# Kernel optimization log

Hardware: AMD Instinct MI355X
Metric: run time of the kernel (lower is better)

## Reference

```python
import jax, jax.numpy as jnp
import numpy as np

SOS = 4998
EOS = 4999
SCALING = 2.0


def setup_inputs() -> dict:
    key = jax.random.key(0)
    ks = jax.random.split(key, 12)
    B, T, E, D, A, C, F, ODIM, L = 32, 1000, 512, 1024, 512, 10, 100, 5000, 100
    s = 0.02
    return {
        "hpad": jax.random.normal(ks[0], (B, T, E), jnp.float32),
        "ys": jax.random.randint(ks[1], (B, L), 0, SOS, jnp.int32),
        # AttLoc params
        "w_enc": jax.random.normal(ks[2], (A, E), jnp.float32) * s,
        "b_enc": jnp.zeros((A,), jnp.float32),
        "w_dec": jax.random.normal(ks[3], (A, D), jnp.float32) * s,
        "w_att": jax.random.normal(ks[4], (A, C), jnp.float32) * s,
        "w_conv": jax.random.normal(ks[5], (C, 1, 2 * F + 1), jnp.float32) * s,  # OIH 1D conv kernel
        "w_gvec": jax.random.normal(ks[6], (1, A), jnp.float32) * s,
        "b_gvec": jnp.zeros((1,), jnp.float32),
        # Decoder params
        "embed": jax.random.normal(ks[7], (ODIM, D), jnp.float32) * s,
        "w_ih": jax.random.normal(ks[8], (4 * D, D + E), jnp.float32) * s,
        "w_hh": jax.random.normal(ks[9], (4 * D, D), jnp.float32) * s,
        "b_ih": jnp.zeros((4 * D,), jnp.float32),
        "b_hh": jnp.zeros((4 * D,), jnp.float32),
        "w_out": jax.random.normal(ks[10], (ODIM, D), jnp.float32) * s,
        "b_out": jnp.zeros((ODIM,), jnp.float32),
    }


def _decode(hpad, ys, w_enc, b_enc, w_dec, w_att, w_conv, w_gvec, b_gvec,
            embed, w_ih, w_hh, b_ih, b_hh, w_out, b_out):
    B, T, E = hpad.shape
    D = w_hh.shape[1]
    F = (w_conv.shape[-1] - 1) // 2
    # ys_in = [sos; y] per utterance (all same length -> already padded)
    ys_in = jnp.concatenate([jnp.full((B, 1), SOS, ys.dtype), ys], axis=1)  # [B, olen]
    eys = embed[ys_in]                                                      # [B, olen, D]
    # pre_compute_enc_h = mlp_enc(enc_h)
    pre = jnp.einsum('bte,ae->bta', hpad, w_enc) + b_enc                    # [B, T, A]
    att0 = jnp.full((B, T), 1.0 / T, hpad.dtype)   # uniform init attention (all hlen == T)
    z0 = jnp.zeros((B, D), hpad.dtype)
    c0 = jnp.zeros((B, D), hpad.dtype)

    def step(carry, ey_i):
        z, c, aw = carry
        # location-aware conv over previous attention weights: [B,1,T] -> [B,C,T]
        conv = jax.lax.conv_general_dilated(aw[:, None, :], w_conv, (1,), [(F, F)],
                                            dimension_numbers=('NCH', 'OIH', 'NCH'))
        att_feat = jnp.einsum('bct,ac->bta', conv, w_att)                   # mlp_att
        dec = (z @ w_dec.T)[:, None, :]                                     # mlp_dec, tiled
        e = jnp.tanh(att_feat + pre + dec) @ w_gvec[0] + b_gvec[0]          # [B, T]
        w = jax.nn.softmax(SCALING * e, axis=1)
        ctx = jnp.einsum('bt,bte->be', w, hpad)                             # [B, E]
        # LSTMCell
        x = jnp.concatenate([ey_i, ctx], axis=1)                            # [B, D+E]
        gates = x @ w_ih.T + b_ih + z @ w_hh.T + b_hh
        i_g, f_g, g_g, o_g = jnp.split(gates, 4, axis=1)
        c_new = jax.nn.sigmoid(f_g) * c + jax.nn.sigmoid(i_g) * jnp.tanh(g_g)
        z_new = jax.nn.sigmoid(o_g) * jnp.tanh(c_new)
        return (z_new, c_new, w), z_new

    _, z_all = jax.lax.scan(step, (z0, c0, att0), jnp.swapaxes(eys, 0, 1))  # [olen, B, D]
    y_all = jnp.einsum('obd,vd->obv', z_all, w_out) + b_out                 # [olen, B, odim]
    return jnp.swapaxes(y_all, 0, 1)                                        # [B, olen, odim]


def reference(hpad, ys, w_enc, b_enc, w_dec, w_att, w_conv, w_gvec, b_gvec,
              embed, w_ih, w_hh, b_ih, b_hh, w_out, b_out):
    return _decode(hpad, ys, w_enc, b_enc, w_dec, w_att, w_conv, w_gvec, b_gvec,
                   embed, w_ih, w_hh, b_ih, b_hh, w_out, b_out)
```

## Files before the change

### kernel.cpp

```cpp
#include <hip/hip_runtime.h>
#include <math.h>

#define B_    32
#define T_    1000
#define E_    512
#define D_    1024
#define A_    512
#define C_    10
#define F_    100
#define ODIM_ 5000
#define OLEN_ 101
#define SOS_  4998

#define OFF_PRE   0u
#define N_PREF    (32u*512u*1000u/2u)
#define OFF_HPB   (OFF_PRE + N_PREF)
#define N_HPBF    (32u*1000u*512u/2u)
#define OFF_DEC   (OFF_HPB + N_HPBF)
#define N_DEC     (32u*512u)
#define OFF_CONV  (OFF_DEC + N_DEC)
#define N_CONVB   (32u*10u*1000u)
#define OFF_AW    (OFF_CONV + N_CONVB)
#define N_AW      (32u*1000u)
#define OFF_S     (OFF_AW + N_AW)
#define N_S       (64u)
#define OFF_CTX   (OFF_S + N_S)
#define N_CTX     (32u*512u)
#define OFF_GP    (OFF_CTX + N_CTX)
#define N_GP      (8u*32u*4096u)
#define OFF_Z     (OFF_GP + N_GP)
#define N_Z       (32u*1024u)
#define OFF_C     (OFF_Z + N_Z)
#define OFF_ZALL  (OFF_C + N_Z)

__device__ __forceinline__ float fast_tanh(float x) {
    float cx = fminf(8.f, fmaxf(-8.f, x));
    float e = __expf(2.f * cx);
    return (e - 1.f) * __builtin_amdgcn_rcpf(e + 1.f);
}
__device__ __forceinline__ float fast_sigmoid(float x) {
    float cx = fminf(30.f, fmaxf(-30.f, x));
    return __builtin_amdgcn_rcpf(1.f + __expf(-cx));
}

__device__ __forceinline__ unsigned bf16rne(float f) {
    unsigned u = __float_as_uint(f);
    return (u + 0x7fffu + ((u >> 16) & 1u)) >> 16;
}
__device__ __forceinline__ unsigned packbf(float lo, float hi) {
    return bf16rne(lo) | (bf16rne(hi) << 16);
}
__device__ __forceinline__ float bflo(unsigned u) { return __uint_as_float(u << 16); }
__device__ __forceinline__ float bfhi(unsigned u) { return __uint_as_float(u & 0xffff0000u); }

__global__ __launch_bounds__(256) void k_init(float* ws) {
    int i = blockIdx.x * 256 + threadIdx.x;
    if (i < (int)N_Z) { ws[OFF_Z + i] = 0.f; ws[OFF_C + i] = 0.f; }
    if (i < (int)N_CTX) ws[OFF_CTX + i] = 0.f;
    if (i < (int)N_AW) ws[OFF_AW + i] = 1.0f;
    if (i < 64) ws[OFF_S + i] = (i >= 32) ? 1000.f : 0.f;
}

__global__ __launch_bounds__(256) void k_hp16(const float* __restrict__ hp, float* ws) {
    uint2* hpb = (uint2*)(ws + OFF_HPB);
    const float4* src = (const float4*)hp;
    for (unsigned i = blockIdx.x * 256 + threadIdx.x; i < 4096000u; i += 4000u * 256u) {
        float4 v = src[i];
        uint2 o;
        o.x = packbf(v.x, v.y);
        o.y = packbf(v.z, v.w);
        hpb[i] = o;
    }
}

__global__ __launch_bounds__(256) void k_pre_t(const float* __restrict__ hp,
                                               const float* __restrict__ we,
                                               const float* __restrict__ be,
                                               float* ws) {
    __shared__ float As[64][68];
    __shared__ float Bs[64][68];
    unsigned short* preb = (unsigned short*)(ws + OFF_PRE);
    int bt = blockIdx.y;
    int b = bt >> 4, tc = bt & 15;
    int t0 = tc * 64;
    int n0 = blockIdx.x * 64;
    int tid = threadIdx.x;
    int tr = tid >> 4, tcl = tid & 15;
    float acc[4][4] = {};
    for (int k0 = 0; k0 < 512; k0 += 64) {
        for (int i = tid; i < 1024; i += 256) {
            int m = i >> 4, kq = (i & 15) << 2;
            int t = t0 + m;
            float4 v = (t < 1000) ? *(const float4*)&hp[((size_t)(b * 1000 + t)) * 512 + k0 + kq]
                                  : make_float4(0.f, 0.f, 0.f, 0.f);
            As[kq + 0][m] = v.x; As[kq + 1][m] = v.y; As[kq + 2][m] = v.z; As[kq + 3][m] = v.w;
            float4 w = *(const float4*)&we[(size_t)(n0 + m) * 512 + k0 + kq];
            Bs[kq + 0][m] = w.x; Bs[kq + 1][m] = w.y; Bs[kq + 2][m] = w.z; Bs[kq + 3][m] = w.w;
        }
        __syncthreads();
        #pragma unroll 16
        for (int kk = 0; kk < 64; ++kk) {
            float4 av = *(const float4*)&As[kk][tr << 2];
            float4 bv = *(const float4*)&Bs[kk][tcl << 2];
            float a[4] = {av.x, av.y, av.z, av.w};
            float bq[4] = {bv.x, bv.y, bv.z, bv.w};
            #pragma unroll
            for (int i = 0; i < 4; i++)
                #pragma unroll
                for (int j = 0; j < 4; j++) acc[i][j] += a[i] * bq[j];
        }
        __syncthreads();
    }
    int tt = t0 + (tr << 2);
    if (tt < 1000) {
        #pragma unroll
        for (int j = 0; j < 4; ++j) {
            int a = n0 + (tcl << 2) + j;
            float bea = be[a];
            uint2 o;
            o.x = packbf(acc[0][j] + bea, acc[1][j] + bea);
            o.y = packbf(acc[2][j] + bea, acc[3][j] + bea);
            *(uint2*)&preb[((size_t)(b * 512 + a)) * 1000 + tt] = o;
        }
    }
}

__global__ __launch_bounds__(256, 2) void k_prep(const float* __restrict__ wdec,
                                                 const float* __restrict__ wconv,
                                                 const float* __restrict__ wih,
                                                 const float* __restrict__ whh,
                                                 const float* __restrict__ embed,
                                                 const int* __restrict__ ys,
                                                 float* ws, int step) {
    int tid = threadIdx.x;
    if (blockIdx.x < 1024) {
        int u = blockIdx.x;
        if (u < 64) ws[OFF_CTX + u * 256 + tid] = 0.f;
        if (u == 64 && tid < 32) ws[OFF_S + (step & 1) * 32 + tid] = 0.f;
        int w = u * 4 + (tid >> 6);
        int lane = tid & 63;
        int a = w >> 3, bg7 = w & 7;
        const float4* wr = (const float4*)(wdec + (size_t)a * 1024);
        float4 w4[4];
        #pragma unroll
        for (int i = 0; i < 4; i++) w4[i] = wr[i * 64 + lane];
        float acc[4] = {0.f, 0.f, 0.f, 0.f};
        #pragma unroll
        for (int bb = 0; bb < 4; ++bb) {
            const float4* zr = (const float4*)(ws + OFF_Z + (size_t)(bg7 * 4 + bb) * 1024);
            #pragma unroll
            for (int i = 0; i < 4; i++) {
                float4 z4 = zr[i * 64 + lane];
                acc[bb] += w4[i].x * z4.x + w4[i].y * z4.y + w4[i].z * z4.z + w4[i].w * z4.w;
            }
        }
        #pragma unroll
        for (int off = 32; off > 0; off >>= 1) {
            acc[0] += __shfl_xor(acc[0], off, 64);
            acc[1] += __shfl_xor(acc[1], off, 64);
            acc[2] += __shfl_xor(acc[2], off, 64);
            acc[3] += __shfl_xor(acc[3], off, 64);
        }
        if (lane == 0) {
            #pragma unroll
            for (int bb = 0; bb < 4; ++bb)
                ws[OFF_DEC + (bg7 * 4 + bb) * 512 + a] = acc[bb];
        }
    } else if (blockIdx.x < 1344) {
        int blk = blockIdx.x - 1024;
        int b = blk / 10, c = blk - b * 10;
        if (tid >= 250) return;
        float invS = __builtin_amdgcn_rcpf(ws[OFF_S + ((step + 1) & 1) * 32 + b]);
        int t = tid * 4;
        const float* ar = ws + OFF_AW + b * 1000;
        const float* wc = wconv + c * 201;
        float a0, a1, a2, a3;
        a0 = (t - 100 >= 0) ? ar[t - 100] : 0.f;
        a1 = (t -  99 >= 0) ? ar[t -  99] : 0.f;
        a2 = (t -  98 >= 0) ? ar[t -  98] : 0.f;
        a3 = (t -  97 >= 0) ? ar[t -  97] : 0.f;
        float c0 = 0.f, c1 = 0.f, c2 = 0.f, c3 = 0.f;
        #pragma unroll 4
        for (int j = 0; j < 201; ++j) {
            float w = wc[j];
            c0 += a0 * w; c1 += a1 * w; c2 += a2 * w; c3 += a3 * w;
            a0 = a1; a1 = a2; a2 = a3;
            int ni = t + j - 96;
            a3 = (ni >= 0 && ni < 1000) ? ar[ni] : 0.f;
        }
        float* o = ws + OFF_CONV + (size_t)(b * 10 + c) * 1000 + t;
        o[0] = c0 * invS; o[1] = c1 * invS; o[2] = c2 * invS; o[3] = c3 * invS;
    } else {
        __shared__ float wlds[32][132];
        __shared__ float xs[32][36];
        int blk = blockIdx.x - 1344;
        int nt = blk & 31, ks = blk >> 5;
        int n0 = nt * 128;
        bool isE = (ks < 4);
        int kloc = isE ? ks * 256 : (ks - 4) * 256;
        int r = tid >> 1, h = tid & 1;
        int bx = tid >> 3, q8 = tid & 7;
        int tok = (step == 0) ? SOS_ : ys[bx * 100 + step - 1];
        const float* xsrc = isE ? (embed + (size_t)tok * 1024 + kloc)
                                : (ws + OFF_Z + (size_t)bx * 1024 + kloc);
        int nq = tid & 31, bq = tid >> 5;
        float acc[4][4] = {};
        for (int kc = 0; kc < 8; ++kc) {
            int koff = kc * 32;
            {
                const float* wrow = isE ? (wih + (size_t)(n0 + r) * 1536 + kloc + koff + h * 16)
                                        : (whh + (size_t)(n0 + r) * 1024 + kloc + koff + h * 16);
                #pragma unroll
                for (int j = 0; j < 4; ++j) {
                    float4 v = *(const float4*)&wrow[j * 4];
                    int kb = h * 16 + j * 4;
                    wlds[kb + 0][r] = v.x; wlds[kb + 1][r] = v.y;
                    wlds[kb + 2][r] = v.z; wlds[kb + 3][r] = v.w;
                }
            }
            {
                float4 v = *(const float4*)&xsrc[koff + q8 * 4];
                xs[q8 * 4 + 0][bx] = v.x; xs[q8 * 4 + 1][bx] = v.y;
                xs[q8 * 4 + 2][bx] = v.z; xs[q8 * 4 + 3][bx] = v.w;
            }
            __syncthreads();
            #pragma unroll 8
            for (int kk = 0; kk < 32; ++kk) {
                float4 wv = *(const float4*)&wlds[kk][nq * 4];
                float4 xv = *(const float4*)&xs[kk][bq * 4];
                float wa[4] = {wv.x, wv.y, wv.z, wv.w};
                float xa[4] = {xv.x, xv.y, xv.z, xv.w};
                #pragma unroll
                for (int i = 0; i < 4; i++)
                    #pragma unroll
                    for (int j = 0; j < 4; j++) acc[i][j] += wa[i] * xa[j];
            }
            __syncthreads();
        }
        float* gp = ws + OFF_GP + (size_t)(ks * 32 + bq * 4) * 4096 + n0 + nq * 4;
        #pragma unroll
        for (int j = 0; j < 4; j++)
            #pragma unroll
            for (int i = 0; i < 4; i++)
                gp[(size_t)j * 4096 + i] = acc[i][j];
    }
}

__global__ __launch_bounds__(512) void k_ectx(const float* __restrict__ watt,
                                              const float* __restrict__ gvec,
                                              const float* __restrict__ bgv,
                                              float* ws, int step) {
    __shared__ float part[1024];
    __shared__ float wsh[128];
    const unsigned short* preb = (const unsigned short*)(ws + OFF_PRE);
    const unsigned short* hpb  = (const unsigned short*)(ws + OFF_HPB);
    int b = blockIdx.x >> 3, tc = blockIdx.x & 7;
    int tbase = tc * 128;
    int tid = threadIdx.x;
    int w = tid >> 6, l = tid & 63;
    int t = tbase + l * 2;
    bool valid = (t < 1000);
    float2 cvv[10];
    const float* convb = ws + OFF_CONV + b * 10000;
    #pragma unroll
    for (int c = 0; c < 10; ++c)
        cvv[c] = valid ? *(const float2*)&convb[c * 1000 + t] : make_float2(0.f, 0.f);
    const float* decb = ws + OFF_DEC + b * 512;
    int a0 = w * 64;
    const unsigned short* pt = preb + ((size_t)(b * 512 + a0)) * 1000 + t;
    float ex = 0.f, ey = 0.f;
    #pragma unroll 8
    for (int a = a0; a < a0 + 64; ++a) {
        unsigned u = valid ? *(const unsigned*)pt : 0u;
        pt += 1000;
        float px = bflo(u), py = bfhi(u);
        float da = decb[a];
        float sx = px + da, sy = py + da;
        const float* wa = watt + a * 10;
        #pragma unroll
        for (int c = 0; c < 10; ++c) {
            float wv = wa[c];
            sx += cvv[c].x * wv; sy += cvv[c].y * wv;
        }
        float gva = gvec[a];
        ex += gva * fast_tanh(sx);
        ey += gva * fast_tanh(sy);
    }
    part[w * 128 + l * 2]     = ex;
    part[w * 128 + l * 2 + 1] = ey;
    __syncthreads();
    float wtil = 0.f;
    if (tid < 128) {
        int tt = tbase + tid;
        float e = 0.f;
        #pragma unroll
        for (int j = 0; j < 8; ++j) e += part[j * 128 + tid];
        if (tt < 1000) {
            wtil = __expf(2.f * (e + bgv[0]));
            ws[OFF_AW + b * 1000 + tt] = wtil;
        }
        wsh[tid] = wtil;
    }
    __syncthreads();
    part[tid] = wtil;
    __syncthreads();
    for (int off = 256; off >= 1; off >>= 1) {
        if (tid < off) part[tid] += part[tid + off];
        __syncthreads();
    }
    if (tid == 0) atomicAdd(&ws[OFF_S + (step & 1) * 32 + b], part[0]);
    int e4 = tid & 127, th = tid >> 7;
    int lt0 = th * 32;
    int ltend = lt0 + 32;
    int tmax = 1000 - tbase; if (ltend > tmax) ltend = tmax;
    float4 acc = make_float4(0.f, 0.f, 0.f, 0.f);
    for (int lt = lt0; lt < ltend; ++lt) {
        float wv = wsh[lt];
        uint2 hu = *(const uint2*)&hpb[((size_t)(b * 1000 + tbase + lt)) * 512 + e4 * 4];
        acc.x += wv * bflo(hu.x); acc.y += wv * bfhi(hu.x);
        acc.z += wv * bflo(hu.y); acc.w += wv * bfhi(hu.y);
    }
    float* cx = ws + OFF_CTX + b * 512 + e4 * 4;
    atomicAdd(cx + 0, acc.x); atomicAdd(cx + 1, acc.y);
    atomicAdd(cx + 2, acc.z); atomicAdd(cx + 3, acc.w);
}

__global__ __launch_bounds__(256, 2) void k_gl(const float* __restrict__ wih,
                                               const float* __restrict__ bih,
                                               const float* __restrict__ bhh,
                                               float* ws, int step) {
    __shared__ float wlds[32][36];
    __shared__ float xs[32][36];
    __shared__ float glb[32][33];
    __shared__ float sinv[32];
    int tid = threadIdx.x;
    int d0 = blockIdx.x * 8;
    if (tid < 32) sinv[tid] = __builtin_amdgcn_rcpf(ws[OFF_S + (step & 1) * 32 + tid]);
    __syncthreads();
    int r = tid >> 3, h = tid & 7;
    int ng_r = (r >> 3) * 1024 + d0 + (r & 7);
    const float* wrow = wih + (size_t)ng_r * 1536 + 1024 + h * 4;
    int bx = tid >> 3, q8 = tid & 7;
    const float* xsrc = ws + OFF_CTX + (size_t)bx * 512 + q8 * 4;
    float xscale = sinv[bx];
    int nq = tid & 15, bq = tid >> 4;
    float acc[2][2] = {};
    for (int kc = 0; kc < 16; ++kc) {
        int k0 = kc * 32;
        {
            float4 v = *(const float4*)&wrow[k0];
            wlds[h * 4 + 0][r] = v.x; wlds[h * 4 + 1][r] = v.y;
            wlds[h * 4 + 2][r] = v.z; wlds[h * 4 + 3][r] = v.w;
        }
        {
            float4 v = *(const float4*)&xsrc[k0];
            xs[q8 * 4 + 0][bx] = v.x * xscale; xs[q8 * 4 + 1][bx] = v.y * xscale;
            xs[q8 * 4 + 2][bx] = v.z * xscale; xs[q8 * 4 + 3][bx] = v.w * xscale;
        }
        __syncthreads();
        #pragma unroll 8
        for (int kk = 0; kk < 32; ++kk) {
            float w0 = wlds[kk][nq * 2], w1 = wlds[kk][nq * 2 + 1];
            float x0 = xs[kk][bq * 2],  x1 = xs[kk][bq * 2 + 1];
            acc[0][0] += w0 * x0; acc[0][1] += w0 * x1;
            acc[1][0] += w1 * x0; acc[1][1] += w1 * x1;
        }
        __syncthreads();
    }
    #pragma unroll
    for (int i = 0; i < 2; ++i) {
        int nl = nq * 2 + i;
        int ng = (nl >> 3) * 1024 + d0 + (nl & 7);
        float bb = bih[ng] + bhh[ng];
        #pragma unroll
        for (int j = 0; j < 2; ++j) {
            int b = bq * 2 + j;
            float s = acc[i][j] + bb;
            #pragma unroll
            for (int sl = 0; sl < 8; ++sl)
                s += ws[OFF_GP + (size_t)(sl * 32 + b) * 4096 + ng];
            glb[nl][b] = s;
        }
    }
    __syncthreads();
    {
        int dl = tid >> 5, b = tid & 31;
        float gi = glb[dl][b];
        float gf = glb[8 + dl][b];
        float gg = glb[16 + dl][b];
        float go = glb[24 + dl][b];
        int id = b * 1024 + d0 + dl;
        float c_old = ws[OFF_C + id];
        float si = fast_sigmoid(gi);
        float sf = fast_sigmoid(gf);
        float so = fast_sigmoid(go);
        float cn = sf * c_old + si * fast_tanh(gg);
        float hh = so * fast_tanh(cn);
        ws[OFF_C + id] = cn;
        ws[OFF_Z + id] = hh;
        ws[OFF_ZALL + ((size_t)step * 32 + b) * 1024 + d0 + dl] = hh;
    }
}

__global__ __launch_bounds__(256) void k_out(const float* __restrict__ zall,
                                             const float* __restrict__ wo,
                                             const float* __restrict__ bo,
                                             float* __restrict__ out) {
    __shared__ float As[64][68];
    __shared__ float Bs[64][68];
    int m0 = blockIdx.y * 64, n0 = blockIdx.x * 64;
    int tid = threadIdx.x;
    int tr = tid >> 4, tc = tid & 15;
    float acc[4][4] = {};
    for (int k0 = 0; k0 < 1024; k0 += 64) {
        for (int i = tid; i < 1024; i += 256) {
            int m = i >> 4, kq = (i & 15) << 2;
            int gm = m0 + m;
            float4 v = (gm < 3232) ? *(const float4*)&zall[(size_t)gm * 1024 + k0 + kq]
                                   : make_float4(0.f, 0.f, 0.f, 0.f);
            As[kq + 0][m] = v.x; As[kq + 1][m] = v.y; As[kq + 2][m] = v.z; As[kq + 3][m] = v.w;
            int gn = n0 + m;
            float4 w = (gn < 5000) ? *(const float4*)&wo[(size_t)gn * 1024 + k0 + kq]
                                   : make_float4(0.f, 0.f, 0.f, 0.f);
            Bs[kq + 0][m] = w.x; Bs[kq + 1][m] = w.y; Bs[kq + 2][m] = w.z; Bs[kq + 3][m] = w.w;
        }
        __syncthreads();
        #pragma unroll 16
        for (int kk = 0; kk < 64; ++kk) {
            float4 av = *(const float4*)&As[kk][tr << 2];
            float4 bv = *(const float4*)&Bs[kk][tc << 2];
            float a[4] = {av.x, av.y, av.z, av.w};
            float b[4] = {bv.x, bv.y, bv.z, bv.w};
            #pragma unroll
            for (int i = 0; i < 4; i++)
                #pragma unroll
                for (int j = 0; j < 4; j++) acc[i][j] += a[i] * b[j];
        }
        __syncthreads();
    }
    #pragma unroll
    for (int i = 0; i < 4; i++) {
        int m = m0 + (tr << 2) + i;
        if (m >= 3232) continue;
        int b = m & 31, o = m >> 5;
        #pragma unroll
        for (int j = 0; j < 4; j++) {
            int v = n0 + (tc << 2) + j;
            if (v < 5000)
                out[((size_t)b * 101 + o) * 5000 + v] = acc[i][j] + bo[v];
        }
    }
}

extern "C" void kernel_launch(void* const* d_in, const int* in_sizes, int n_in,
                              void* d_out, int out_size, void* d_ws, size_t ws_size,
                              hipStream_t stream) {
    const float* hpad   = (const float*)d_in[0];
    const int*   ys     = (const int*)d_in[1];
    const float* w_enc  = (const float*)d_in[2];
    const float* b_enc  = (const float*)d_in[3];
    const float* w_dec  = (const float*)d_in[4];
    const float* w_att  = (const float*)d_in[5];
    const float* w_conv = (const float*)d_in[6];
    const float* w_gvec = (const float*)d_in[7];
    const float* b_gvec = (const float*)d_in[8];
    const float* embed  = (const float*)d_in[9];
    const float* w_ih   = (const float*)d_in[10];
    const float* w_hh   = (const float*)d_in[11];
    const float* b_ih   = (const float*)d_in[12];
    const float* b_hh   = (const float*)d_in[13];
    const float* w_out  = (const float*)d_in[14];
    const float* b_out  = (const float*)d_in[15];
    float* ws  = (float*)d_ws;
    float* out = (float*)d_out;

    k_init<<<128, 256, 0, stream>>>(ws);
    k_hp16<<<4000, 256, 0, stream>>>(hpad, ws);
    k_pre_t<<<dim3(8, 512), 256, 0, stream>>>(hpad, w_enc, b_enc, ws);

    for (int step = 0; step < OLEN_; ++step) {
        k_prep<<<1600, 256, 0, stream>>>(w_dec, w_conv, w_ih, w_hh, embed, ys, ws, step);
        k_ectx<<<256, 512, 0, stream>>>(w_att, w_gvec, b_gvec, ws, step);
        k_gl<<<128, 256, 0, stream>>>(w_ih, b_ih, b_hh, ws, step);
    }

    k_out<<<dim3(79, 51), 256, 0, stream>>>(ws + OFF_ZALL, w_out, b_out, out);
}
```

Before: 10.38 ms.

## Stage attention weights in LDS and split LSTM gate kernel across more blocks

k_ectx now copies w_att, w_gvec and the decoder projection for the batch row into shared memory once per block, and the inner loop reads them as float4 from LDS instead of scalar global loads. Its launch bounds now request two blocks per CU. k_gl now handles 4 hidden units per block instead of 8 and launches 256 blocks, so the serial per-step gate GEMV is spread over more CUs. The cost is redundant ctx loading per block and half the threads idling in the LSTM cell update.

Result: no change. 10.19 ms (-1.9%).

```diff
diff --git a/kernel.cpp b/kernel.cpp
--- a/kernel.cpp
+++ b/kernel.cpp
@@ -246,10 +246,11 @@
     }
 }
 
-__global__ __launch_bounds__(512) void k_ectx(const float* __restrict__ watt,
-                                              const float* __restrict__ gvec,
-                                              const float* __restrict__ bgv,
-                                              float* ws, int step) {
+__global__ __launch_bounds__(512, 2) void k_ectx(const float* __restrict__ watt,
+                                                 const float* __restrict__ gvec,
+                                                 const float* __restrict__ bgv,
+                                                 float* ws, int step) {
+    __shared__ float sa[512 * 12];
     __shared__ float part[1024];
     __shared__ float wsh[128];
     const unsigned short* preb = (const unsigned short*)(ws + OFF_PRE);
@@ -257,6 +258,15 @@
     int b = blockIdx.x >> 3, tc = blockIdx.x & 7;
     int tbase = tc * 128;
     int tid = threadIdx.x;
+    {
+        const float* wrow = watt + tid * 10;
+        float* d = sa + tid * 12;
+        #pragma unroll
+        for (int c = 0; c < 10; ++c) d[c] = wrow[c];
+        d[10] = gvec[tid];
+        d[11] = ws[OFF_DEC + b * 512 + tid];
+    }
+    __syncthreads();
     int w = tid >> 6, l = tid & 63;
     int t = tbase + l * 2;
     bool valid = (t < 1000);
@@ -265,7 +275,6 @@
     #pragma unroll
     for (int c = 0; c < 10; ++c)
         cvv[c] = valid ? *(const float2*)&convb[c * 1000 + t] : make_float2(0.f, 0.f);
-    const float* decb = ws + OFF_DEC + b * 512;
     int a0 = w * 64;
     const unsigned short* pt = preb + ((size_t)(b * 512 + a0)) * 1000 + t;
     float ex = 0.f, ey = 0.f;
@@ -273,18 +282,24 @@
     for (int a = a0; a < a0 + 64; ++a) {
         unsigned u = valid ? *(const unsigned*)pt : 0u;
         pt += 1000;
+        const float4* sp = (const float4*)(sa + a * 12);
+        float4 w0 = sp[0];
+        float4 w1 = sp[1];
+        float4 w2 = sp[2];
         float px = bflo(u), py = bfhi(u);
-        float da = decb[a];
-        float sx = px + da, sy = py + da;
-        const float* wa = watt + a * 10;
-        #pragma unroll
-        for (int c = 0; c < 10; ++c) {
-            float wv = wa[c];
-            sx += cvv[c].x * wv; sy += cvv[c].y * wv;
-        }
-        float gva = gvec[a];
-        ex += gva * fast_tanh(sx);
-        ey += gva * fast_tanh(sy);
+        float sx = px + w2.w, sy = py + w2.w;
+        sx += cvv[0].x * w0.x; sy += cvv[0].y * w0.x;
+        sx += cvv[1].x * w0.y; sy += cvv[1].y * w0.y;
+        sx += cvv[2].x * w0.z; sy += cvv[2].y * w0.z;
+        sx += cvv[3].x * w0.w; sy += cvv[3].y * w0.w;
+        sx += cvv[4].x * w1.x; sy += cvv[4].y * w1.x;
+        sx += cvv[5].x * w1.y; sy += cvv[5].y * w1.y;
+        sx += cvv[6].x * w1.z; sy += cvv[6].y * w1.z;
+        sx += cvv[7].x * w1.w; sy += cvv[7].y * w1.w;
+        sx += cvv[8].x * w2.x; sy += cvv[8].y * w2.x;
+        sx += cvv[9].x * w2.y; sy += cvv[9].y * w2.y;
+        ex += w2.z * fast_tanh(sx);
+        ey += w2.z * fast_tanh(sy);
     }
     part[w * 128 + l * 2]     = ex;
     part[w * 128 + l * 2 + 1] = ey;
@@ -329,28 +344,28 @@
                                                const float* __restrict__ bih,
                                                const float* __restrict__ bhh,
                                                float* ws, int step) {
-    __shared__ float wlds[32][36];
-    __shared__ float xs[32][36];
-    __shared__ float glb[32][33];
+    __shared__ float wlds[32][20];
+    __shared__ float xs[32][33];
+    __shared__ float glb[16][33];
     __shared__ float sinv[32];
     int tid = threadIdx.x;
-    int d0 = blockIdx.x * 8;
+    int d0 = blockIdx.x * 4;
     if (tid < 32) sinv[tid] = __builtin_amdgcn_rcpf(ws[OFF_S + (step & 1) * 32 + tid]);
     __syncthreads();
-    int r = tid >> 3, h = tid & 7;
-    int ng_r = (r >> 3) * 1024 + d0 + (r & 7);
-    const float* wrow = wih + (size_t)ng_r * 1536 + 1024 + h * 4;
+    int r = tid >> 4, h = tid & 15;
+    int ng_r = (r >> 2) * 1024 + d0 + (r & 3);
+    const float* wrow = wih + (size_t)ng_r * 1536 + 1024 + h * 2;
     int bx = tid >> 3, q8 = tid & 7;
     const float* xsrc = ws + OFF_CTX + (size_t)bx * 512 + q8 * 4;
     float xscale = sinv[bx];
-    int nq = tid & 15, bq = tid >> 4;
-    float acc[2][2] = {};
+    int nq = tid & 7, bq = tid >> 3;
+    float acc[2] = {0.f, 0.f};
     for (int kc = 0; kc < 16; ++kc) {
         int k0 = kc * 32;
         {
-            float4 v = *(const float4*)&wrow[k0];
-            wlds[h * 4 + 0][r] = v.x; wlds[h * 4 + 1][r] = v.y;
-            wlds[h * 4 + 2][r] = v.z; wlds[h * 4 + 3][r] = v.w;
+            float2 v = *(const float2*)&wrow[k0];
+            wlds[h * 2 + 0][r] = v.x;
+            wlds[h * 2 + 1][r] = v.y;
         }
         {
             float4 v = *(const float4*)&xsrc[k0];
@@ -361,34 +376,29 @@
         #pragma unroll 8
         for (int kk = 0; kk < 32; ++kk) {
             float w0 = wlds[kk][nq * 2], w1 = wlds[kk][nq * 2 + 1];
-            float x0 = xs[kk][bq * 2],  x1 = xs[kk][bq * 2 + 1];
-            acc[0][0] += w0 * x0; acc[0][1] += w0 * x1;
-            acc[1][0] += w1 * x0; acc[1][1] += w1 * x1;
+            float x  = xs[kk][bq];
+            acc[0] += w0 * x;
+            acc[1] += w1 * x;
         }
         __syncthreads();
     }
     #pragma unroll
     for (int i = 0; i < 2; ++i) {
         int nl = nq * 2 + i;
-        int ng = (nl >> 3) * 1024 + d0 + (nl & 7);
-        float bb = bih[ng] + bhh[ng];
-        #pragma unroll
-        for (int j = 0; j < 2; ++j) {
-            int b = bq * 2 + j;
-            float s = acc[i][j] + bb;
-            #pragma unroll
-            for (int sl = 0; sl < 8; ++sl)
-                s += ws[OFF_GP + (size_t)(sl * 32 + b) * 4096 + ng];
-            glb[nl][b] = s;
-        }
-    }
-    __syncthreads();
-    {
+        int ng = (nl >> 2) * 1024 + d0 + (nl & 3);
+        float s = acc[i] + bih[ng] + bhh[ng];
+        #pragma unroll
+        for (int sl = 0; sl < 8; ++sl)
+            s += ws[OFF_GP + (size_t)(sl * 32 + bq) * 4096 + ng];
+        glb[nl][bq] = s;
+    }
+    __syncthreads();
+    if (tid < 128) {
         int dl = tid >> 5, b = tid & 31;
         float gi = glb[dl][b];
-        float gf = glb[8 + dl][b];
-        float gg = glb[16 + dl][b];
-        float go = glb[24 + dl][b];
+        float gf = glb[4 + dl][b];
+        float gg = glb[8 + dl][b];
+        float go = glb[12 + dl][b];
         int id = b * 1024 + d0 + dl;
         float c_old = ws[OFF_C + id];
         float si = fast_sigmoid(gi);
@@ -481,7 +491,7 @@
     for (int step = 0; step < OLEN_; ++step) {
         k_prep<<<1600, 256, 0, stream>>>(w_dec, w_conv, w_ih, w_hh, embed, ys, ws, step);
         k_ectx<<<256, 512, 0, stream>>>(w_att, w_gvec, b_gvec, ws, step);
-        k_gl<<<128, 256, 0, stream>>>(w_ih, b_ih, b_hh, ws, step);
+        k_gl<<<256, 256, 0, stream>>>(w_ih, b_ih, b_hh, ws, step);
     }
 
     k_out<<<dim3(79, 51), 256, 0, stream>>>(ws + OFF_ZALL, w_out, b_out, out);
```
